# Performance work log

Hardware: AMD Instinct MI355X
Metric: run time of the kernel (lower is better)

The kernel has to match this reference:

```python
import jax, jax.numpy as jnp
import numpy as np

B, O, T = 32, 256, 1024
D_OBJ = 512      # obj_input_dim
D_PRED = 512     # predicate_input_dim
HID = 512        # hidden_dim
P_OUT = 512      # predicate_output_dim
OBJ_OUT = 512    # object_output_dim
N_PRED_TYPES = 50
ORIGINAL_EDGE = 0
TRANSITIVE_EDGE = 1


def setup_inputs() -> dict:
    key = jax.random.key(0)
    ks = jax.random.split(key, 16)

    def kaiming(k, fan_in, fan_out):
        return jax.random.normal(k, (fan_in, fan_out), jnp.float32) * np.sqrt(2.0 / fan_in)

    n1_in = 2 * D_OBJ + D_PRED            # 1536
    n1_out = 2 * HID + P_OUT              # 1536
    return {
        "obj_vecs": jax.random.normal(ks[0], (B, O, D_OBJ), jnp.float32),
        "pred_vecs": jax.random.normal(ks[1], (B, T, D_PRED), jnp.float32),
        "W1a": kaiming(ks[2], n1_in, HID), "b1a": jnp.zeros((HID,), jnp.float32),
        "W1b": kaiming(ks[3], HID, n1_out), "b1b": jnp.zeros((n1_out,), jnp.float32),
        "W2a": kaiming(ks[4], HID, HID), "b2a": jnp.zeros((HID,), jnp.float32),
        "W2b": kaiming(ks[5], HID, OBJ_OUT), "b2b": jnp.zeros((OBJ_OUT,), jnp.float32),
        "pt_weights": jax.random.normal(ks[6], (N_PRED_TYPES,), jnp.float32),
        "edges": jax.random.randint(ks[7], (B, T, 2), 0, O, jnp.int32),
        "pred_indicators": jax.random.randint(ks[8], (B, T), 0, 2, jnp.int32).astype(bool),
        "triplet_type": jax.random.randint(ks[9], (B, T), 0, 2, jnp.int32),
        "predicate_ids": jax.random.randint(ks[10], (B, T), 0, N_PRED_TYPES, jnp.int32),
    }


def reference(obj_vecs, pred_vecs, W1a, b1a, W1b, b1b, W2a, b2a, W2b, b2b,
              pt_weights, edges, pred_indicators, triplet_type, predicate_ids):
    s_idx = edges[:, :, 0]  # [B,T]
    o_idx = edges[:, :, 1]

    # gather subject/object vectors: [B,T,D]
    cur_s = jnp.take_along_axis(obj_vecs, s_idx[:, :, None], axis=1)
    cur_o = jnp.take_along_axis(obj_vecs, o_idx[:, :, None], axis=1)
    cur_t = jnp.concatenate([cur_s, pred_vecs, cur_o], axis=-1)  # [B,T,2D+Dp]

    # net1: Linear-ReLU-Linear-ReLU
    h = jax.nn.relu(cur_t @ W1a + b1a)
    new_t = jax.nn.relu(h @ W1b + b1b)  # [B,T,2*HID+P_OUT]

    # confidence weighting
    pt_pred = jax.nn.sigmoid(pt_weights)  # [N_PRED_TYPES]
    conf = ((triplet_type == ORIGINAL_EDGE).astype(jnp.float32)
            + (triplet_type == TRANSITIVE_EDGE).astype(jnp.float32) * pt_pred[predicate_ids])  # [B,T]
    new_t = new_t * conf[:, :, None]

    new_s = new_t[:, :, :HID]
    new_p = new_t[:, :, HID:HID + P_OUT]
    new_o = new_t[:, :, HID + P_OUT:]

    mask = pred_indicators.astype(jnp.float32)  # [B,T]

    def pool_one(si, oi, sv, ov, cf, m):
        # masked scatter-add (equivalent to torch boolean-masked scatter_add)
        sums = (jax.ops.segment_sum(sv * m[:, None], si, num_segments=O)
                + jax.ops.segment_sum(ov * m[:, None], oi, num_segments=O))  # [O,HID]
        w = cf * m
        counts = (jax.ops.segment_sum(w, si, num_segments=O)
                  + jax.ops.segment_sum(w, oi, num_segments=O))  # [O]
        nz = counts > 0
        return jnp.where(nz[:, None], sums / jnp.where(nz, counts, 1.0)[:, None], sums)

    pooled = jax.vmap(pool_one)(s_idx, o_idx, new_s, new_o, conf, mask)  # [B,O,HID]

    # net2: Linear-ReLU-Linear-ReLU
    h2 = jax.nn.relu(pooled @ W2a + b2a)
    new_obj = jax.nn.relu(h2 @ W2b + b2b)  # [B,O,OBJ_OUT]

    return new_obj, new_p
```

## Files before the change

### kernel.cpp

```cpp
#include <hip/hip_runtime.h>
#include <hip/hip_bf16.h>
#include <cstdint>
#include <cstddef>

#define DEV __device__ __forceinline__

typedef __attribute__((ext_vector_type(8))) short  s8v;
typedef __attribute__((ext_vector_type(4))) float  f4v;
typedef __attribute__((ext_vector_type(4))) uint32_t u4v;

DEV unsigned short f2bf(float x) {
  union { float f; uint32_t u; } v; v.f = x;
  uint32_t u = v.u + 0x7FFFu + ((v.u >> 16) & 1u);
  return (unsigned short)(u >> 16);
}
DEV uint32_t cvtpk2(float lo, float hi) {
  uint32_t r;
  asm("v_cvt_pk_bf16_f32 %0, %1, %2" : "=v"(r) : "v"(lo), "v"(hi));
  return r;
}
DEV unsigned short f2bf_fast(float x) { return (unsigned short)cvtpk2(x, 0.f); }
DEV float bf2f(unsigned short b) {
  union { uint32_t u; float f; } v; v.u = ((uint32_t)b) << 16;
  return v.f;
}

DEV void async_copy16(void* lds, const void* g) {
  typedef __attribute__((address_space(3))) uint32_t lds_t;
  typedef const __attribute__((address_space(1))) uint32_t g_t;
  __builtin_amdgcn_global_load_lds((g_t*)g, (lds_t*)lds, 16, 0, 0);
}

#define WAITV4()    asm volatile("s_waitcnt vmcnt(4)" ::: "memory")
#define WAITV0()    asm volatile("s_waitcnt vmcnt(0)" ::: "memory")
#define MEMFENCE()  asm volatile("" ::: "memory")

constexpr int Bc = 32, Oc = 256, Tc = 1024;
constexpr int BM = 128, BN = 128, BK = 64;
constexpr int CSR_CAP = 46;

DEV void swz_mn(int nyb, int* mb, int* nb) {
  const int nwg = gridDim.x * gridDim.y;
  const int w   = blockIdx.x + blockIdx.y * gridDim.x;
  const int cpx = nwg >> 3;
  const int s   = (w & 7) * cpx + (w >> 3);
  *mb = s / nyb;
  *nb = s % nyb;
}

__global__ __launch_bounds__(256)
void cvt_k(const float* __restrict__ in, unsigned short* __restrict__ outp, int n8)
{
  const int i = blockIdx.x * 256 + threadIdx.x;
  if (i >= n8) return;
  const f4v v0 = *(const f4v*)(in + (size_t)i * 8);
  const f4v v1 = *(const f4v*)(in + (size_t)i * 8 + 4);
  u4v pk;
  pk.x = cvtpk2(v0.x, v0.y);
  pk.y = cvtpk2(v0.z, v0.w);
  pk.z = cvtpk2(v1.x, v1.y);
  pk.w = cvtpk2(v1.z, v1.w);
  *(u4v*)(outp + (size_t)i * 8) = pk;
}

#define READ_A(QM, DST) do {                                                    \
    _Pragma("unroll")                                                           \
    for (int i = 0; i < 4; ++i) {                                               \
      const int row = wm * 128 + ((QM) * 4 + i) * 16 + (lane & 15);             \
      _Pragma("unroll")                                                         \
      for (int kk = 0; kk < 2; ++kk) {                                          \
        const int c = kk * 4 + (lane >> 4);                                     \
        DST[i][kk] = *(const s8v*)(Ab_ + row * 128 + ((c ^ (row & 7)) << 4));   \
      }                                                                         \
    }                                                                           \
  } while (0)

#define READ_B(QN, DST) do {                                                    \
    _Pragma("unroll")                                                           \
    for (int j = 0; j < 2; ++j) {                                               \
      const int row = wn * 64 + ((QN) * 2 + j) * 16 + (lane & 15);              \
      _Pragma("unroll")                                                         \
      for (int kk = 0; kk < 2; ++kk) {                                          \
        const int c = kk * 4 + (lane >> 4);                                     \
        DST[j][kk] = *(const s8v*)(Bb_ + row * 128 + ((c ^ (row & 7)) << 4));   \
      }                                                                         \
    }                                                                           \
  } while (0)

#define SYNC_MFMA(QM, QN, AF, BF) do {                                          \
    MEMFENCE();                                                                 \
    __builtin_amdgcn_s_barrier();                                               \
    asm volatile("s_waitcnt lgkmcnt(0)" ::: "memory");                          \
    __builtin_amdgcn_sched_barrier(0);                                          \
    __builtin_amdgcn_s_setprio(1);                                              \
    _Pragma("unroll")                                                           \
    for (int i = 0; i < 4; ++i)                                                 \
      _Pragma("unroll")                                                         \
      for (int j = 0; j < 2; ++j)                                               \
        _Pragma("unroll")                                                       \
        for (int kk = 0; kk < 2; ++kk)                                          \
          acc[(QM) * 4 + i][(QN) * 2 + j] =                                     \
            __builtin_amdgcn_mfma_f32_16x16x32_bf16(                            \
              AF[i][kk], BF[j][kk], acc[(QM) * 4 + i][(QN) * 2 + j], 0, 0, 0);  \
    __builtin_amdgcn_s_setprio(0);                                              \
  } while (0)

#define ENDPHASE() do { MEMFENCE(); __builtin_amdgcn_s_barrier(); } while (0)

#define KTILE_BODY() do {                                                       \
    const int par = t & 1, px = par ^ 1;                                        \
    const char* Ab_ = smem + par * 65536;                                       \
    const char* Bb_ = Ab_ + 32768;                                              \
    const bool s1 = (t + 1 < nk), s2 = (t + 2 < nk);                            \
                                                                        \
    READ_A(0, af); READ_B(0, bf0);                                              \
    if (s1) stageA(px, 1, t + 1);                                               \
    SYNC_MFMA(0, 0, af, bf0);                                                   \
    ENDPHASE();                                                                 \
                                                                        \
    READ_B(1, bf1);                                                             \
    if (s1) stageB(px, 1, t + 1);                                               \
    SYNC_MFMA(0, 1, af, bf1);                                                   \
    ENDPHASE();                                                                 \
                                                                        \
    READ_A(1, af);                                                              \
    if (s2) stageA(par, 0, t + 2);                                              \
    SYNC_MFMA(1, 1, af, bf1);                                                   \
    ENDPHASE();                                                                 \
                                                                        \
    if (s2) stageB(par, 0, t + 2);                                              \
    SYNC_MFMA(1, 0, af, bf0);                                                   \
    if (s2) { WAITV4(); } else if (s1) { WAITV0(); }                            \
    ENDPHASE();                                                                 \
  } while (0)

__global__ __launch_bounds__(512, 2)
void gemm8g_k(const unsigned short* __restrict__ objb,
              const unsigned short* __restrict__ predb,
              const int* __restrict__ edges,
              const unsigned short* __restrict__ Bt,
              const float* __restrict__ bias,
              unsigned short* __restrict__ outp)
{
  __shared__ __align__(16) char smem[131072];

  const int tid = threadIdx.x, lane = tid & 63, wave = tid >> 6;
  const int wm = wave >> 2, wn = wave & 3;
  int mb, nb; swz_mn(gridDim.y, &mb, &nb);
  const int m0 = mb * 256, n0 = nb * 256;
  const int rl  = tid >> 3;
  const int cs8 = ((lane & 7) ^ (lane >> 3)) * 8;
  const int rB0 = (rl >> 5) * 64 + (rl & 31);

  uint32_t offS[4], offP[4], offO[4];
  #pragma unroll
  for (int c2 = 0; c2 < 4; ++c2) {
    const int r = (c2 >> 1) * 128 + (c2 & 1) * 64 + rl;
    const int m = m0 + r;
    const int ob = (m >> 10) * Oc;
    offS[c2] = (uint32_t)((ob + edges[2 * m])     * 1024 + cs8 * 2);
    offO[c2] = (uint32_t)((ob + edges[2 * m + 1]) * 1024 + cs8 * 2);
    offP[c2] = (uint32_t)(m * 1024 + cs8 * 2);
  }
  const unsigned short* srcB = Bt + (size_t)(n0 + rB0) * 1536 + cs8;

  auto stageA = [&](int p, int qm, int kt) {
    const int reg = kt >> 3;
    const uint32_t koff = (uint32_t)(kt & 7) * 128u;
    #pragma unroll
    for (int s = 0; s < 2; ++s) {
      const int c2 = s * 2 + qm;
      const char* src;
      if (reg == 0)      src = (const char*)objb  + offS[c2] + koff;
      else if (reg == 1) src = (const char*)predb + offP[c2] + koff;
      else               src = (const char*)objb  + offO[c2] + koff;
      async_copy16(smem + p * 65536 + ((s * 128 + qm * 64 + wave * 8) << 7), src);
    }
  };
  auto stageB = [&](int p, int qn, int kt) {
    #pragma unroll
    for (int s = 0; s < 2; ++s)
      async_copy16(smem + p * 65536 + 32768 +
                     ((s * 128 + qn * 32 + (wave >> 2) * 64 + (wave & 3) * 8) << 7),
                   srcB + (size_t)(s * 128 + qn * 32) * 1536 + kt * 64);
  };

  f4v acc[8][4] = {};
  s8v af[4][2], bf0[2][2], bf1[2][2];
  constexpr int nk = 24;

  stageA(0, 0, 0); stageB(0, 0, 0); stageA(0, 1, 0); stageB(0, 1, 0);
  stageA(1, 0, 1); stageB(1, 0, 1);
  WAITV4();
  MEMFENCE();
  __builtin_amdgcn_s_barrier();

  for (int t = 0; t < nk; ++t) KTILE_BODY();

  const int cn = lane & 15, rq4 = (lane >> 4) * 4;
  #pragma unroll
  for (int f = 0; f < 8; ++f) {
    const int gr0 = m0 + wm * 128 + f * 16 + rq4;
    #pragma unroll
    for (int g = 0; g < 4; ++g) {
      const int gc = n0 + wn * 64 + g * 16 + cn;
      const float bv = bias[gc];
      #pragma unroll
      for (int r = 0; r < 4; ++r) {
        float val = acc[f][g][r] + bv;
        val = val > 0.f ? val : 0.f;
        outp[(size_t)(gr0 + r) * 512 + gc] = f2bf_fast(val);
      }
    }
  }
}

__global__ __launch_bounds__(256)
void gemm2_k(const unsigned short* __restrict__ Abf,
             const unsigned short* __restrict__ Bt,
             const float* __restrict__ bias,
             const float* __restrict__ conf,
             unsigned short* __restrict__ out_bf,
             float* __restrict__ out_f32,
             unsigned short* __restrict__ out_bf2,
             int M, int N, int K)
{
  __shared__ __align__(16) char smem[BM * BK * 2 + BN * BK * 2];
  char* As = smem;
  char* Bs = smem + BM * BK * 2;

  const int tid  = threadIdx.x;
  const int lane = tid & 63;
  const int wave = tid >> 6;
  const int wm = wave >> 1, wn = wave & 1;
  int mb, nb; swz_mn(gridDim.y, &mb, &nb);
  const int m0 = mb * BM;
  const int n0 = nb * BN;

  f4v acc[4][4] = {};

  for (int k0 = 0; k0 < K; k0 += BK) {
    {
      const int r8 = lane >> 3;
      const int cs = (lane & 7) ^ r8;
      const unsigned short* src = Bt + (size_t)(n0 + wave * 32 + r8) * K + k0 + cs * 8;
      #pragma unroll
      for (int i = 0; i < 4; ++i)
        async_copy16(Bs + (wave * 32 + i * 8) * 128, src + (size_t)i * 8 * K);
      const unsigned short* srca = Abf + (size_t)(m0 + wave * 32 + r8) * K + k0 + cs * 8;
      #pragma unroll
      for (int i = 0; i < 4; ++i)
        async_copy16(As + (wave * 32 + i * 8) * 128, srca + (size_t)i * 8 * K);
    }
    __syncthreads();

    #pragma unroll
    for (int kk = 0; kk < 2; ++kk) {
      s8v af[4], bfv[4];
      #pragma unroll
      for (int i = 0; i < 4; ++i) {
        const int row = wm * 64 + i * 16 + (lane & 15);
        const int c = kk * 4 + (lane >> 4);
        af[i] = *(const s8v*)(As + row * 128 + ((c ^ (row & 7)) << 4));
      }
      #pragma unroll
      for (int j = 0; j < 4; ++j) {
        const int row = wn * 64 + j * 16 + (lane & 15);
        const int c = kk * 4 + (lane >> 4);
        bfv[j] = *(const s8v*)(Bs + row * 128 + ((c ^ (row & 7)) << 4));
      }
      #pragma unroll
      for (int i = 0; i < 4; ++i)
        #pragma unroll
        for (int j = 0; j < 4; ++j)
          acc[i][j] = __builtin_amdgcn_mfma_f32_16x16x32_bf16(af[i], bfv[j], acc[i][j], 0, 0, 0);
    }
    __syncthreads();
  }

  const int cn = lane & 15, rq4 = (lane >> 4) * 4;
  #pragma unroll
  for (int i = 0; i < 4; ++i) {
    const int gr0 = m0 + wm * 64 + i * 16 + rq4;
    #pragma unroll
    for (int j = 0; j < 4; ++j) {
      const int gc = n0 + wn * 64 + j * 16 + cn;
      const float bv = bias[gc];
      #pragma unroll
      for (int r = 0; r < 4; ++r) {
        float val = acc[i][j][r] + bv;
        val = val > 0.f ? val : 0.f;
        const int gr = gr0 + r;
        val *= conf[gr];
        if (gc < 512)        out_bf [(size_t)gr * 512 + gc]          = f2bf_fast(val);
        else if (gc < 1024)  out_f32[(size_t)gr * 512 + (gc - 512)]  = val;
        else                 out_bf2[(size_t)gr * 512 + (gc - 1024)] = f2bf_fast(val);
      }
    }
  }
}

template<int EPI>
__global__ __launch_bounds__(256)
void gemm_k(const unsigned short* __restrict__ Abf,
            const unsigned short* __restrict__ Bt,
            const float* __restrict__ bias,
            unsigned short* __restrict__ out_bf,
            float* __restrict__ out_f32,
            int M, int N, int K)
{
  __shared__ __align__(16) char smem[BM * BK * 2 + BN * BK * 2];
  char* As = smem;
  char* Bs = smem + BM * BK * 2;

  const int tid  = threadIdx.x;
  const int lane = tid & 63;
  const int wave = tid >> 6;
  const int wm = wave >> 1, wn = wave & 1;
  int mb, nb; swz_mn(gridDim.y, &mb, &nb);
  const int m0 = mb * BM;
  const int n0 = nb * BN;

  f4v acc[4][4] = {};

  for (int k0 = 0; k0 < K; k0 += BK) {
    {
      const int r8 = lane >> 3;
      const int cs = (lane & 7) ^ r8;
      const unsigned short* src = Bt + (size_t)(n0 + wave * 32 + r8) * K + k0 + cs * 8;
      #pragma unroll
      for (int i = 0; i < 4; ++i)
        async_copy16(Bs + (wave * 32 + i * 8) * 128, src + (size_t)i * 8 * K);
      const unsigned short* srca = Abf + (size_t)(m0 + wave * 32 + r8) * K + k0 + cs * 8;
      #pragma unroll
      for (int i = 0; i < 4; ++i)
        async_copy16(As + (wave * 32 + i * 8) * 128, srca + (size_t)i * 8 * K);
    }
    __syncthreads();

    #pragma unroll
    for (int kk = 0; kk < 2; ++kk) {
      s8v af[4], bfv[4];
      #pragma unroll
      for (int i = 0; i < 4; ++i) {
        const int row = wm * 64 + i * 16 + (lane & 15);
        const int c = kk * 4 + (lane >> 4);
        af[i] = *(const s8v*)(As + row * 128 + ((c ^ (row & 7)) << 4));
      }
      #pragma unroll
      for (int j = 0; j < 4; ++j) {
        const int row = wn * 64 + j * 16 + (lane & 15);
        const int c = kk * 4 + (lane >> 4);
        bfv[j] = *(const s8v*)(Bs + row * 128 + ((c ^ (row & 7)) << 4));
      }
      #pragma unroll
      for (int i = 0; i < 4; ++i)
        #pragma unroll
        for (int j = 0; j < 4; ++j)
          acc[i][j] = __builtin_amdgcn_mfma_f32_16x16x32_bf16(af[i], bfv[j], acc[i][j], 0, 0, 0);
    }
    __syncthreads();
  }

  const int cn = lane & 15, rq4 = (lane >> 4) * 4;
  #pragma unroll
  for (int i = 0; i < 4; ++i) {
    const int gr0 = m0 + wm * 64 + i * 16 + rq4;
    #pragma unroll
    for (int j = 0; j < 4; ++j) {
      const int gc = n0 + wn * 64 + j * 16 + cn;
      const float bv = bias[gc];
      #pragma unroll
      for (int r = 0; r < 4; ++r) {
        float val = acc[i][j][r] + bv;
        val = val > 0.f ? val : 0.f;
        const int gr = gr0 + r;
        if (EPI == 0) out_bf[(size_t)gr * N + gc] = f2bf_fast(val);
        else          out_f32[(size_t)gr * N + gc] = val;
      }
    }
  }
}

__global__ void tcvt_k(const float* __restrict__ W, unsigned short* __restrict__ Wt,
                       int K, int N)
{
  __shared__ float tile[32][33];
  const int k0 = blockIdx.x * 32, n0 = blockIdx.y * 32;
  const int tx = threadIdx.x, ty = threadIdx.y;
  #pragma unroll
  for (int i = 0; i < 32; i += 8)
    tile[ty + i][tx] = W[(size_t)(k0 + ty + i) * N + (n0 + tx)];
  __syncthreads();
  #pragma unroll
  for (int i = 0; i < 32; i += 8)
    Wt[(size_t)(n0 + ty + i) * K + (k0 + tx)] = f2bf(tile[tx][ty + i]);
}

__global__ void detect_k(const unsigned char* __restrict__ mb, int* __restrict__ flag)
{
  __shared__ int any;
  if (threadIdx.x == 0) any = 0;
  __syncthreads();
  int local = 0;
  for (int i = threadIdx.x; i < Bc * Tc; i += 256)
    if ((i & 3) && mb[i]) local = 1;
  if (local) atomicOr(&any, 1);
  __syncthreads();
  if (threadIdx.x == 0) *flag = any;
}

__global__ void prep_k(const int* __restrict__ tt, const int* __restrict__ pid,
                       const float* __restrict__ ptw, const int* __restrict__ edges,
                       const void* __restrict__ mask, const int* __restrict__ u8flag,
                       float* __restrict__ conf, int* __restrict__ se, int* __restrict__ oe)
{
  const int m = blockIdx.x * 256 + threadIdx.x;
  const int t = tt[m];
  float c = 0.f;
  if (t == 0) c = 1.f;
  else if (t == 1) c = 1.f / (1.f + expf(-ptw[pid[m]]));
  conf[m] = c;
  bool mk;
  if (*u8flag) mk = ((const unsigned char*)mask)[m] != 0;
  else         mk = ((const int*)mask)[m] != 0;
  se[m] = mk ? edges[2 * m]     : -1;
  oe[m] = mk ? edges[2 * m + 1] : -1;
}

__global__ __launch_bounds__(256)
void csr2_k(const int* __restrict__ se, const int* __restrict__ oe,
            int* __restrict__ deg, int* __restrict__ slot)
{
  const int wid  = blockIdx.x * 4 + (threadIdx.x >> 6);
  const int b    = wid >> 8;
  const int u    = wid & 255;
  const int lane = threadIdx.x & 63;
  const int mb   = b * Tc;
  int* sl = slot + (size_t)wid * CSR_CAP;
  const unsigned long long lt = (1ull << lane) - 1ull;
  int cnt = 0;
  #pragma unroll 4
  for (int c = 0; c < 16; ++c) {
    const int t = c * 64 + lane;
    const int s = se[mb + t];
    const int o = oe[mb + t];
    const unsigned long long ms = __ballot(s == u);
    const unsigned long long mo = __ballot(o == u);
    if (s == u) {
      const int pos = cnt + (int)__popcll(ms & lt);
      if (pos < CSR_CAP) sl[pos] = 2 * t;
    }
    cnt += (int)__popcll(ms);
    if (o == u) {
      const int pos = cnt + (int)__popcll(mo & lt);
      if (pos < CSR_CAP) sl[pos] = 2 * t + 1;
    }
    cnt += (int)__popcll(mo);
  }
  if (lane == 0) deg[wid] = cnt < CSR_CAP ? cnt : CSR_CAP;
}

__global__ __launch_bounds__(256)
void pool2_k(const unsigned short* __restrict__ S, const unsigned short* __restrict__ Ov,
             const int* __restrict__ deg, const int* __restrict__ slot,
             const float* __restrict__ conf,
             unsigned short* __restrict__ pooled)
{
  const int bo = blockIdx.x;
  const int b  = bo >> 8;
  const int u  = threadIdx.x;
  const int d  = deg[bo];
  const int* sl = slot + (size_t)bo * CSR_CAP;
  float a0 = 0.f, a1 = 0.f, w = 0.f;
  for (int i = 0; i < d; ++i) {
    const int e = sl[i];
    const int t = e >> 1;
    const unsigned short* row = ((e & 1) ? Ov : S) + ((size_t)(b * Tc + t)) * 512;
    const uint32_t pr = *(const uint32_t*)(row + 2 * u);
    a0 += bf2f((unsigned short)pr);
    a1 += bf2f((unsigned short)(pr >> 16));
    w  += conf[b * Tc + t];
  }
  const float denom = (w > 0.f) ? w : 1.f;
  const size_t ob = (size_t)bo * 512;
  *(uint32_t*)(pooled + ob + 2 * u) = cvtpk2(a0 / denom, a1 / denom);
}

extern "C" void kernel_launch(void* const* d_in, const int* in_sizes, int n_in,
                              void* d_out, int out_size, void* d_ws, size_t ws_size,
                              hipStream_t stream)
{
  const float* obj  = (const float*)d_in[0];
  const float* pred = (const float*)d_in[1];
  const float* W1a  = (const float*)d_in[2];
  const float* b1a  = (const float*)d_in[3];
  const float* W1b  = (const float*)d_in[4];
  const float* b1b  = (const float*)d_in[5];
  const float* W2a  = (const float*)d_in[6];
  const float* b2a  = (const float*)d_in[7];
  const float* W2b  = (const float*)d_in[8];
  const float* b2b  = (const float*)d_in[9];
  const float* ptw  = (const float*)d_in[10];
  const int*   edges = (const int*)d_in[11];
  const void*  mask  = d_in[12];
  const int*   tt    = (const int*)d_in[13];
  const int*   pid   = (const int*)d_in[14];
  float* out = (float*)d_out;

  char* ws = (char*)d_ws;
  unsigned short* W1at = (unsigned short*)(ws + 0);
  unsigned short* W1bt = (unsigned short*)(ws + 1572864);
  unsigned short* W2at = (unsigned short*)(ws + 3145728);
  unsigned short* W2bt = (unsigned short*)(ws + 3670016);
  int* deg  = (int*)(ws + 0);
  int* slot = (int*)(ws + 32768);
  unsigned short* h    = (unsigned short*)(ws + 4194304);
  unsigned short* pooled = h;
  unsigned short* h2   = (unsigned short*)(ws + 12582912);
  unsigned short* news = (unsigned short*)(ws + 37748736);
  unsigned short* newo = (unsigned short*)(ws + 71303168);
  unsigned short* objb = news;
  unsigned short* predb = (unsigned short*)(ws + 46137344);
  float* conf = (float*)(ws + 104857600);
  int*   se   = (int*)(ws + 104988672);
  int*   oe   = (int*)(ws + 105119744);
  int* u8flag = (int*)(ws + 105250816);

  tcvt_k<<<dim3(48, 16), dim3(32, 8), 0, stream>>>(W1a, W1at, 1536, 512);
  tcvt_k<<<dim3(16, 48), dim3(32, 8), 0, stream>>>(W1b, W1bt, 512, 1536);
  tcvt_k<<<dim3(16, 16), dim3(32, 8), 0, stream>>>(W2a, W2at, 512, 512);
  tcvt_k<<<dim3(16, 16), dim3(32, 8), 0, stream>>>(W2b, W2bt, 512, 512);

  cvt_k<<<2048, 256, 0, stream>>>(obj,  objb,  Bc * Oc * 512 / 8);
  cvt_k<<<8192, 256, 0, stream>>>(pred, predb, Bc * Tc * 512 / 8);

  detect_k<<<1, 256, 0, stream>>>((const unsigned char*)mask, u8flag);
  prep_k<<<128, 256, 0, stream>>>(tt, pid, ptw, edges, mask, u8flag, conf, se, oe);

  gemm8g_k<<<dim3(128, 2), 512, 0, stream>>>(objb, predb, edges, W1at, b1a, h);

  csr2_k<<<2048, 256, 0, stream>>>(se, oe, deg, slot);

  gemm2_k<<<dim3(256, 12), 256, 0, stream>>>(
      h, W1bt, b1b, conf, news, out + 4194304, newo, 32768, 1536, 512);

  pool2_k<<<Bc * Oc, 256, 0, stream>>>(news, newo, deg, slot, conf, pooled);

  gemm_k<0><<<dim3(64, 4), 256, 0, stream>>>(
      pooled, W2at, b2a, h2, nullptr, 8192, 512, 512);

  gemm_k<2><<<dim3(64, 4), 256, 0, stream>>>(
      h2, W2bt, b2b, nullptr, out, 8192, 512, 512);
}
```

Measured before the change: 256.9 us.

## Compact masked triplets and run subject/object GEMM only on active rows

Measured after the change: 280.4 us. 1.09x slower.

```diff
diff --git a/kernel.cpp b/kernel.cpp
--- a/kernel.cpp
+++ b/kernel.cpp
@@ -215,15 +215,15 @@
   }
 }
 
+template<int EPI>
 __global__ __launch_bounds__(256)
-void gemm2_k(const unsigned short* __restrict__ Abf,
-             const unsigned short* __restrict__ Bt,
-             const float* __restrict__ bias,
-             const float* __restrict__ conf,
-             unsigned short* __restrict__ out_bf,
-             float* __restrict__ out_f32,
-             unsigned short* __restrict__ out_bf2,
-             int M, int N, int K)
+void gemm_k(const unsigned short* __restrict__ Abf,
+            const unsigned short* __restrict__ Bt,
+            const float* __restrict__ bias,
+            const float* __restrict__ conf,
+            unsigned short* __restrict__ out_bf,
+            float* __restrict__ out_f32,
+            int M, int N, int K)
 {
   __shared__ __align__(16) char smem[BM * BK * 2 + BN * BK * 2];
   char* As = smem;
@@ -291,24 +291,30 @@
         float val = acc[i][j][r] + bv;
         val = val > 0.f ? val : 0.f;
         const int gr = gr0 + r;
-        val *= conf[gr];
-        if (gc < 512)        out_bf [(size_t)gr * 512 + gc]          = f2bf_fast(val);
-        else if (gc < 1024)  out_f32[(size_t)gr * 512 + (gc - 512)]  = val;
-        else                 out_bf2[(size_t)gr * 512 + (gc - 1024)] = f2bf_fast(val);
+        if (EPI == 0) out_bf[(size_t)gr * N + gc] = f2bf_fast(val);
+        else if (EPI == 2) out_f32[(size_t)gr * N + gc] = val;
+        else { out_f32[(size_t)gr * N + gc] = val * conf[gr]; }
       }
     }
   }
 }
 
-template<int EPI>
 __global__ __launch_bounds__(256)
-void gemm_k(const unsigned short* __restrict__ Abf,
-            const unsigned short* __restrict__ Bt,
-            const float* __restrict__ bias,
-            unsigned short* __restrict__ out_bf,
-            float* __restrict__ out_f32,
-            int M, int N, int K)
-{
+void gemm2so_k(const unsigned short* __restrict__ h,
+               const int* __restrict__ torig,
+               const float* __restrict__ confc,
+               const unsigned short* __restrict__ W1bt,
+               const float* __restrict__ b1b,
+               const int* __restrict__ minfo,
+               unsigned short* __restrict__ news_c,
+               unsigned short* __restrict__ newo_c)
+{
+  const int Mp = minfo[1];
+  int mb, nb; swz_mn(gridDim.y, &mb, &nb);
+  const int m0 = mb * BM;
+  if (m0 >= Mp) return;
+  const int Mr = minfo[0];
+
   __shared__ __align__(16) char smem[BM * BK * 2 + BN * BK * 2];
   char* As = smem;
   char* Bs = smem + BM * BK * 2;
@@ -317,25 +323,30 @@
   const int lane = tid & 63;
   const int wave = tid >> 6;
   const int wm = wave >> 1, wn = wave & 1;
-  int mb, nb; swz_mn(gridDim.y, &mb, &nb);
-  const int m0 = mb * BM;
   const int n0 = nb * BN;
+  const int r8 = lane >> 3;
+  const int cs8 = ((lane & 7) ^ r8) * 8;
+
+  const unsigned short* aP[4];
+  #pragma unroll
+  for (int i = 0; i < 4; ++i) {
+    int m = m0 + wave * 32 + i * 8 + r8;
+    m = m < Mr ? m : Mr - 1;
+    aP[i] = h + (size_t)torig[m] * 512 + cs8;
+  }
+  const int nrow0 = (nb < 4) ? n0 : n0 + 512;
+  const unsigned short* bsrc = W1bt + (size_t)(nrow0 + wave * 32 + r8) * 512 + cs8;
 
   f4v acc[4][4] = {};
 
-  for (int k0 = 0; k0 < K; k0 += BK) {
-    {
-      const int r8 = lane >> 3;
-      const int cs = (lane & 7) ^ r8;
-      const unsigned short* src = Bt + (size_t)(n0 + wave * 32 + r8) * K + k0 + cs * 8;
-      #pragma unroll
-      for (int i = 0; i < 4; ++i)
-        async_copy16(Bs + (wave * 32 + i * 8) * 128, src + (size_t)i * 8 * K);
-      const unsigned short* srca = Abf + (size_t)(m0 + wave * 32 + r8) * K + k0 + cs * 8;
-      #pragma unroll
-      for (int i = 0; i < 4; ++i)
-        async_copy16(As + (wave * 32 + i * 8) * 128, srca + (size_t)i * 8 * K);
-    }
+  for (int kt = 0; kt < 8; ++kt) {
+    const int kin = kt * 64;
+    #pragma unroll
+    for (int i = 0; i < 4; ++i)
+      async_copy16(Bs + (wave * 32 + i * 8) * 128, bsrc + (size_t)(i * 8) * 512 + kin);
+    #pragma unroll
+    for (int i = 0; i < 4; ++i)
+      async_copy16(As + (wave * 32 + i * 8) * 128, aP[i] + kin);
     __syncthreads();
 
     #pragma unroll
@@ -362,21 +373,24 @@
     __syncthreads();
   }
 
+  const float* bb = b1b + ((nb < 4) ? n0 : 512 + n0);
+  unsigned short* outp = (nb < 4) ? news_c : newo_c;
+  const int c0 = (nb & 3) * 128;
   const int cn = lane & 15, rq4 = (lane >> 4) * 4;
   #pragma unroll
   for (int i = 0; i < 4; ++i) {
     const int gr0 = m0 + wm * 64 + i * 16 + rq4;
     #pragma unroll
     for (int j = 0; j < 4; ++j) {
-      const int gc = n0 + wn * 64 + j * 16 + cn;
-      const float bv = bias[gc];
+      const int lc = wn * 64 + j * 16 + cn;
+      const float bv = bb[lc];
       #pragma unroll
       for (int r = 0; r < 4; ++r) {
+        const int gr = gr0 + r;
         float val = acc[i][j][r] + bv;
         val = val > 0.f ? val : 0.f;
-        const int gr = gr0 + r;
-        if (EPI == 0) out_bf[(size_t)gr * N + gc] = f2bf_fast(val);
-        else          out_f32[(size_t)gr * N + gc] = val;
+        val *= confc[gr < Mr ? gr : 0];
+        if (gr < Mr) outp[(size_t)gr * 512 + c0 + lc] = f2bf_fast(val);
       }
     }
   }
@@ -413,7 +427,8 @@
 __global__ void prep_k(const int* __restrict__ tt, const int* __restrict__ pid,
                        const float* __restrict__ ptw, const int* __restrict__ edges,
                        const void* __restrict__ mask, const int* __restrict__ u8flag,
-                       float* __restrict__ conf, int* __restrict__ se, int* __restrict__ oe)
+                       float* __restrict__ conf, int* __restrict__ se,
+                       int* __restrict__ oe)
 {
   const int m = blockIdx.x * 256 + threadIdx.x;
   const int t = tt[m];
@@ -426,6 +441,57 @@
   else         mk = ((const int*)mask)[m] != 0;
   se[m] = mk ? edges[2 * m]     : -1;
   oe[m] = mk ? edges[2 * m + 1] : -1;
+}
+
+__global__ __launch_bounds__(1024)
+void scan1_k(const int* __restrict__ se, int* __restrict__ bsum)
+{
+  const int m = blockIdx.x * 1024 + threadIdx.x;
+  const unsigned long long bal = __ballot(se[m] >= 0);
+  __shared__ int wc[16];
+  if ((threadIdx.x & 63) == 0) wc[threadIdx.x >> 6] = (int)__popcll(bal);
+  __syncthreads();
+  if (threadIdx.x == 0) {
+    int s = 0;
+    #pragma unroll
+    for (int i = 0; i < 16; ++i) s += wc[i];
+    bsum[blockIdx.x] = s;
+  }
+}
+
+__global__ void scan2_k(const int* __restrict__ bsum, int* __restrict__ boff,
+                        int* __restrict__ minfo)
+{
+  if (threadIdx.x == 0) {
+    int s = 0;
+    for (int i = 0; i < 32; ++i) { boff[i] = s; s += bsum[i]; }
+    minfo[0] = s;
+    minfo[1] = (s + 127) & ~127;
+  }
+}
+
+__global__ __launch_bounds__(1024)
+void scan3_k(const int* __restrict__ se, const int* __restrict__ boff,
+             const float* __restrict__ conf,
+             int* __restrict__ torig, int* __restrict__ cmap,
+             float* __restrict__ confc)
+{
+  const int m = blockIdx.x * 1024 + threadIdx.x;
+  const int lane = threadIdx.x & 63, w = threadIdx.x >> 6;
+  const bool mv = se[m] >= 0;
+  const unsigned long long bal = __ballot(mv);
+  __shared__ int wc[16];
+  if (lane == 0) wc[w] = (int)__popcll(bal);
+  __syncthreads();
+  int woff = 0;
+  for (int i = 0; i < w; ++i) woff += wc[i];
+  if (mv) {
+    const int c = boff[blockIdx.x] + woff +
+                  (int)__popcll(bal & ((1ull << lane) - 1ull));
+    torig[c] = m;
+    cmap[m]  = c;
+    confc[c] = conf[m];
+  }
 }
 
 __global__ __launch_bounds__(256)
@@ -464,7 +530,7 @@
 __global__ __launch_bounds__(256)
 void pool2_k(const unsigned short* __restrict__ S, const unsigned short* __restrict__ Ov,
              const int* __restrict__ deg, const int* __restrict__ slot,
-             const float* __restrict__ conf,
+             const float* __restrict__ conf, const int* __restrict__ cmap,
              unsigned short* __restrict__ pooled)
 {
   const int bo = blockIdx.x;
@@ -476,7 +542,8 @@
   for (int i = 0; i < d; ++i) {
     const int e = sl[i];
     const int t = e >> 1;
-    const unsigned short* row = ((e & 1) ? Ov : S) + ((size_t)(b * Tc + t)) * 512;
+    const int c = cmap[b * Tc + t];
+    const unsigned short* row = ((e & 1) ? Ov : S) + (size_t)c * 512;
     const uint32_t pr = *(const uint32_t*)(row + 2 * u);
     a0 += bf2f((unsigned short)pr);
     a1 += bf2f((unsigned short)(pr >> 16));
@@ -527,6 +594,14 @@
   int*   oe   = (int*)(ws + 105119744);
   int* u8flag = (int*)(ws + 105250816);
 
+  char* sout = (char*)d_out;
+  int*   torig = (int*)(sout + 0);
+  int*   cmap  = (int*)(sout + 131072);
+  float* confc = (float*)(sout + 262144);
+  int*   bsum  = (int*)(sout + 393216);
+  int*   boff  = (int*)(sout + 393344);
+  int*   minfo = (int*)(sout + 393472);
+
   tcvt_k<<<dim3(48, 16), dim3(32, 8), 0, stream>>>(W1a, W1at, 1536, 512);
   tcvt_k<<<dim3(16, 48), dim3(32, 8), 0, stream>>>(W1b, W1bt, 512, 1536);
   tcvt_k<<<dim3(16, 16), dim3(32, 8), 0, stream>>>(W2a, W2at, 512, 512);
@@ -538,18 +613,25 @@
   detect_k<<<1, 256, 0, stream>>>((const unsigned char*)mask, u8flag);
   prep_k<<<128, 256, 0, stream>>>(tt, pid, ptw, edges, mask, u8flag, conf, se, oe);
 
+  scan1_k<<<32, 1024, 0, stream>>>(se, bsum);
+  scan2_k<<<1, 64, 0, stream>>>(bsum, boff, minfo);
+  scan3_k<<<32, 1024, 0, stream>>>(se, boff, conf, torig, cmap, confc);
+
   gemm8g_k<<<dim3(128, 2), 512, 0, stream>>>(objb, predb, edges, W1at, b1a, h);
 
   csr2_k<<<2048, 256, 0, stream>>>(se, oe, deg, slot);
 
-  gemm2_k<<<dim3(256, 12), 256, 0, stream>>>(
-      h, W1bt, b1b, conf, news, out + 4194304, newo, 32768, 1536, 512);
-
-  pool2_k<<<Bc * Oc, 256, 0, stream>>>(news, newo, deg, slot, conf, pooled);
+  gemm_k<3><<<dim3(256, 4), 256, 0, stream>>>(
+      h, W1bt + 512 * 512, b1b + 512, conf, nullptr, out + 4194304, 32768, 512, 512);
+
+  gemm2so_k<<<dim3(256, 8), 256, 0, stream>>>(
+      h, torig, confc, W1bt, b1b, minfo, news, newo);
+
+  pool2_k<<<Bc * Oc, 256, 0, stream>>>(news, newo, deg, slot, conf, cmap, pooled);
 
   gemm_k<0><<<dim3(64, 4), 256, 0, stream>>>(
-      pooled, W2at, b2a, h2, nullptr, 8192, 512, 512);
+      pooled, W2at, b2a, nullptr, h2, nullptr, 8192, 512, 512);
 
   gemm_k<2><<<dim3(64, 4), 256, 0, stream>>>(
-      h2, W2bt, b2b, nullptr, out, 8192, 512, 512);
-}
+      h2, W2bt, b2b, nullptr, nullptr, out, 8192, 512, 512);
+}
```
